# Kernel optimization log

Measured on AMD Instinct MI355X. Metric: run time of the kernel, lower is better.

The kernel has to match this reference:

```python
import jax, jax.numpy as jnp
import numpy as np

LN_EPS = 1e-5
N_HEADS = 8

def _layernorm(x, g, b):
    mu = jnp.mean(x, axis=-1, keepdims=True)
    var = jnp.var(x, axis=-1, keepdims=True)
    return (x - mu) * jax.lax.rsqrt(var + LN_EPS) * g + b

def _posenc(seqlen, d_model, dtype):
    den = jnp.exp(-jnp.arange(0, d_model, 2, dtype=dtype) * (np.log(10000.0) / d_model))
    pos = jnp.arange(seqlen, dtype=dtype)[:, None]  # [S,1]
    pe = jnp.zeros((seqlen, d_model), dtype=dtype)
    pe = pe.at[:, 0::2].set(jnp.sin(pos * den))
    pe = pe.at[:, 1::2].set(jnp.cos(pos * den)[:, : d_model // 2])
    return pe  # [S,d]

def setup_inputs() -> dict:
    key = jax.random.key(0)
    ks = jax.random.split(key, 12)
    B, S, V, D, F, L, DL = 64, 256, 16, 512, 2048, 6, 256
    s = 0.05
    return {
        "src_pad": jax.random.normal(ks[0], (B, S, V), jnp.float32),
        "emb_w": jax.random.normal(ks[1], (D, V), jnp.float32) * s,
        "emb_b": jnp.zeros((D,), jnp.float32),
        "qkv_w": jax.random.normal(ks[2], (L, 3 * D, D), jnp.float32) * s,
        "qkv_b": jnp.zeros((L, 3 * D), jnp.float32),
        "out_w": jax.random.normal(ks[3], (L, D, D), jnp.float32) * s,
        "out_b": jnp.zeros((L, D), jnp.float32),
        "ff1_w": jax.random.normal(ks[4], (L, F, D), jnp.float32) * s,
        "ff1_b": jnp.zeros((L, F), jnp.float32),
        "ff2_w": jax.random.normal(ks[5], (L, D, F), jnp.float32) * s,
        "ff2_b": jnp.zeros((L, D), jnp.float32),
        "ln1_g": jnp.ones((L, D), jnp.float32),
        "ln1_b": jnp.zeros((L, D), jnp.float32),
        "ln2_g": jnp.ones((L, D), jnp.float32),
        "ln2_b": jnp.zeros((L, D), jnp.float32),
        "lat_w": jax.random.normal(ks[6], (DL, S * D), jnp.float32) * 0.005,
        "lat_b": jnp.zeros((DL,), jnp.float32),
        "head_w": jax.random.normal(ks[7], (1, DL), jnp.float32) * s,
        "head_b": jnp.zeros((1,), jnp.float32),
    }

def reference(src_pad, emb_w, emb_b, qkv_w, qkv_b, out_w, out_b,
              ff1_w, ff1_b, ff2_w, ff2_b, ln1_g, ln1_b, ln2_g, ln2_b,
              lat_w, lat_b, head_w, head_b):
    B, S, V = src_pad.shape
    D = emb_w.shape[0]
    L = qkv_w.shape[0]
    H = N_HEADS
    dh = D // H
    # batched replacement of the per-token Python-loop embedding
    x = jnp.einsum('bsv,dv->bsd', src_pad, emb_w) + emb_b
    x = x + _posenc(S, D, x.dtype)  # dropout is identity at eval
    scale = 1.0 / np.sqrt(dh)
    for l in range(L):  # post-norm PyTorch TransformerEncoderLayer, relu FFN
        qkv = jnp.einsum('bsd,ed->bse', x, qkv_w[l]) + qkv_b[l]  # [B,S,3D]
        q, k, v = jnp.split(qkv, 3, axis=-1)
        q = q.reshape(B, S, H, dh).transpose(0, 2, 1, 3)
        k = k.reshape(B, S, H, dh).transpose(0, 2, 1, 3)
        v = v.reshape(B, S, H, dh).transpose(0, 2, 1, 3)
        attn = jax.nn.softmax(jnp.einsum('bhqd,bhkd->bhqk', q, k) * scale, axis=-1)
        o = jnp.einsum('bhqk,bhkd->bhqd', attn, v).transpose(0, 2, 1, 3).reshape(B, S, D)
        o = jnp.einsum('bsd,ed->bse', o, out_w[l]) + out_b[l]
        x = _layernorm(x + o, ln1_g[l], ln1_b[l])
        h = jax.nn.relu(jnp.einsum('bsd,fd->bsf', x, ff1_w[l]) + ff1_b[l])
        h = jnp.einsum('bsf,df->bsd', h, ff2_w[l]) + ff2_b[l]
        x = _layernorm(x + h, ln2_g[l], ln2_b[l])
    mem = x.reshape(B, S * D) @ lat_w.T + lat_b  # [B, d_latent]
    pred = jax.nn.sigmoid(mem @ head_w.T + head_b)  # [B,1]
    return pred
```

## Files before the change

### kernel.cpp

```cpp
#include <hip/hip_runtime.h>
#include <hip/hip_bf16.h>
#include <cstdint>

#define DEV static __device__ __forceinline__

typedef __attribute__((ext_vector_type(8))) short bf16x8;
typedef __attribute__((ext_vector_type(4))) float f32x4;

DEV unsigned short f2bf(float f) {
  union { float f; unsigned u; } c; c.f = f;
  unsigned u = c.u;
  return (unsigned short)((u + 0x7fffu + ((u >> 16) & 1u)) >> 16);
}
DEV float bf2f(unsigned short h) {
  union { unsigned u; float f; } c; c.u = ((unsigned)h) << 16; return c.f;
}
DEV float bflo(unsigned u) { union { unsigned u; float f; } c; c.u = u << 16; return c.f; }
DEV float bfhi(unsigned u) { union { unsigned u; float f; } c; c.u = u & 0xffff0000u; return c.f; }
DEV unsigned pack_bf16(float a, float b) {
  union { float f; unsigned u; } ca, cb; ca.f = a; cb.f = b;
  return __builtin_amdgcn_perm(cb.u + 0x8000u, ca.u + 0x8000u, 0x07060302u);
}

#define ASYNC_COPY16(gsrc, ldst)                                                      \
  __builtin_amdgcn_global_load_lds(                                                   \
      (const __attribute__((address_space(1))) void*)(unsigned long long)(gsrc),      \
      (__attribute__((address_space(3))) void*)(unsigned int)(unsigned long long)(ldst), \
      16, 0, 0)

__global__ void cvt4_kernel(const float* __restrict__ s, unsigned short* __restrict__ d) {
  size_t i = ((size_t)blockIdx.x * 256 + threadIdx.x) * 4;
  float4 v = *(const float4*)(s + i);
  d[i + 0] = f2bf(v.x);
  d[i + 1] = f2bf(v.y);
  d[i + 2] = f2bf(v.z);
  d[i + 3] = f2bf(v.w);
}

__global__ void embed_kernel(const float* __restrict__ src,
                             const float* __restrict__ emb_w,
                             const float* __restrict__ emb_b,
                             unsigned short* __restrict__ xb) {
  const int bs = blockIdx.x;
  const int d = threadIdx.x;
  const int s = bs & 255;
  __shared__ float sv[16];
  if (d < 16) sv[d] = src[(size_t)bs * 16 + d];
  __syncthreads();
  const float* wr = emb_w + (size_t)d * 16;
  float acc = emb_b[d];
#pragma unroll
  for (int v = 0; v < 16; v++) acc += sv[v] * wr[v];
  const float den = __expf(-(float)(d & ~1) * (9.2103403719761836f / 512.f));
  const float arg = (float)s * den;
  acc += (d & 1) ? __cosf(arg) : __sinf(arg);
  xb[(size_t)bs * 512 + d] = f2bf(acc);
}

template <int BM, int RELU, int OUT_BF16, int ADD_RES>
__global__ __launch_bounds__(512, 2) void gemm_pipe(
    const unsigned short* __restrict__ A,
    const unsigned short* __restrict__ B,
    const float* __restrict__ bias,
    const unsigned short* __restrict__ res,
    float* __restrict__ Cf,
    unsigned short* __restrict__ Cb,
    int M, int N, int K) {
  constexpr int BN = 256;
  constexpr int MT = BM / 32;
  constexpr int NT = 4;
  constexpr int NLA = BM / 64;
  constexpr int NL = NLA + 4;
  __shared__ unsigned short lds[2][(BM + BN) * 64];

  const int tid = threadIdx.x;
  const int lane = tid & 63;
  const int w = tid >> 6;
  const int wmi = w >> 2;
  const int wni = w & 3;
  const int r16 = lane & 15;
  const int quad = lane >> 4;
  const int rsw = r16 & 7;
  const int m0 = blockIdx.x * BM;
  const int n0 = blockIdx.y * BN;

  const int srow = tid >> 3;
  const int scol = ((tid & 7) ^ (srow & 7)) * 8;
  const unsigned short* gA = A + (size_t)(m0 + srow) * K + scol;
  const unsigned short* gB = B + (size_t)(n0 + srow) * K + scol;

#define STG(i, bufi, kc)                                                        \
  do {                                                                          \
    if ((i) < NLA)                                                              \
      ASYNC_COPY16(gA + (size_t)((i) * 64) * K + (kc),                          \
                   &lds[(bufi)][((i) * 64 + w * 8) * 64]);                      \
    else                                                                        \
      ASYNC_COPY16(gB + (size_t)(((i) - NLA) * 64) * K + (kc),                  \
                   &lds[(bufi)][(BM + ((i) - NLA) * 64 + w * 8) * 64]);         \
  } while (0)

  f32x4 acc[MT][NT] = {};

#pragma unroll
  for (int i = 0; i < NL; ++i) STG(i, 0, 0);

  const int NK = K >> 6;
  for (int kt = 0; kt < NK; ++kt) {
    const int buf = kt & 1;
    asm volatile("s_waitcnt vmcnt(0)" ::: "memory");
    __builtin_amdgcn_s_barrier();
    const unsigned short* As = &lds[buf][0];
    const unsigned short* Bs = &lds[buf][BM * 64];
    const int doStage = (kt + 1 < NK);
    const int kc = (kt + 1) << 6;
    const int sb = buf ^ 1;
    bf16x8 aR[MT];
#pragma unroll
    for (int kh = 0; kh < 2; ++kh) {
#pragma unroll
      for (int nh = 0; nh < 2; ++nh) {
        const int ph = kh * 2 + nh;
        const int ko = ((kh * 4 + quad) ^ rsw) * 8;
        if (nh == 0) {
#pragma unroll
          for (int m = 0; m < MT; ++m)
            aR[m] = *(const bf16x8*)(As + (wmi * (MT * 16) + m * 16 + r16) * 64 + ko);
        }
        bf16x8 bR[2];
#pragma unroll
        for (int j = 0; j < 2; ++j)
          bR[j] = *(const bf16x8*)(Bs + (wni * 64 + (nh * 2 + j) * 16 + r16) * 64 + ko);
        if (doStage) {
          if (2 * ph < NL) STG(2 * ph, sb, kc);
          if (2 * ph + 1 < NL) STG(2 * ph + 1, sb, kc);
        }
        __builtin_amdgcn_s_barrier();
        asm volatile("s_waitcnt lgkmcnt(0)" ::: "memory");
        __builtin_amdgcn_s_setprio(1);
#pragma unroll
        for (int m = 0; m < MT; ++m)
#pragma unroll
          for (int j = 0; j < 2; ++j)
            acc[m][nh * 2 + j] = __builtin_amdgcn_mfma_f32_16x16x32_bf16(
                bR[j], aR[m], acc[m][nh * 2 + j], 0, 0, 0);
        __builtin_amdgcn_s_setprio(0);
        __builtin_amdgcn_s_barrier();
      }
    }
  }
#undef STG

  const int mb = m0 + wmi * (MT * 16) + r16;
  const int nb = n0 + wni * 64 + quad * 4;
#pragma unroll
  for (int j = 0; j < NT; ++j) {
    const int n = nb + j * 16;
    const float4 bv = *(const float4*)(bias + n);
#pragma unroll
    for (int i = 0; i < MT; ++i) {
      const size_t off = (size_t)(mb + i * 16) * N + n;
      float4 v;
      v.x = acc[i][j][0] + bv.x;
      v.y = acc[i][j][1] + bv.y;
      v.z = acc[i][j][2] + bv.z;
      v.w = acc[i][j][3] + bv.w;
      if (ADD_RES) {
        const uint2 ru = *(const uint2*)(res + off);
        v.x += bflo(ru.x); v.y += bfhi(ru.x);
        v.z += bflo(ru.y); v.w += bfhi(ru.y);
      }
      if (RELU) {
        v.x = fmaxf(v.x, 0.f); v.y = fmaxf(v.y, 0.f);
        v.z = fmaxf(v.z, 0.f); v.w = fmaxf(v.w, 0.f);
      }
      if (OUT_BF16) {
        uint2 u;
        u.x = pack_bf16(v.x, v.y);
        u.y = pack_bf16(v.z, v.w);
        *(uint2*)(Cb + off) = u;
      } else {
        *(float4*)(Cf + off) = v;
      }
    }
  }
}

__global__ __launch_bounds__(256, 2) void attn_fused(
    const unsigned short* __restrict__ qkv,
    unsigned short* __restrict__ O) {
  __shared__ unsigned short Vt[64 * 264];
  __shared__ unsigned short Pl[32 * 264];
  __shared__ float redM[4][32];
  __shared__ float redS[4][32];
  const int tid = threadIdx.x;
  const int lane = tid & 63;
  const int w = tid >> 6;
  const int r16 = lane & 15;
  const int quad = lane >> 4;
  const int h = blockIdx.x & 7;
  const int b = blockIdx.x >> 3;

  {
    const int kp = w * 32 + (lane & 31);
    const int dhalf = lane >> 5;
    const unsigned short* vbase =
        qkv + (size_t)(b * 256 + 2 * kp) * 1536 + 1024 + h * 64;
    unsigned* dst = (unsigned*)Vt;
#pragma unroll
    for (int t = 0; t < 4; t++) {
      const int dc = dhalf + 2 * t;
      const uint4 a = *(const uint4*)(vbase + dc * 8);
      const uint4 bb = *(const uint4*)(vbase + 1536 + dc * 8);
      const unsigned* ap = (const unsigned*)&a;
      const unsigned* bp = (const unsigned*)&bb;
#pragma unroll
      for (int i = 0; i < 4; i++) {
        const unsigned lo = ap[i], hi = bp[i];
        dst[(dc * 8 + 2 * i) * 132 + kp] = (lo & 0xffffu) | (hi << 16);
        dst[(dc * 8 + 2 * i + 1) * 132 + kp] = (lo >> 16) | (hi & 0xffff0000u);
      }
    }
  }
  __syncthreads();

  const unsigned short* krow =
      qkv + (size_t)(b * 256 + r16) * 1536 + 512 + h * 64 + quad * 8;
  const unsigned short* qrow =
      qkv + (size_t)(b * 256 + r16) * 1536 + h * 64 + quad * 8;

  for (int qt = 0; qt < 8; qt++) {
    const int q0 = qt * 32;
    f32x4 acc[4][2] = {};
    bf16x8 bQ0[2], bQ1[2];
#pragma unroll
    for (int nt = 0; nt < 2; nt++) {
      const unsigned short* qp = qrow + (size_t)(q0 + nt * 16) * 1536;
      bQ0[nt] = *(const bf16x8*)(qp);
      bQ1[nt] = *(const bf16x8*)(qp + 32);
    }
#pragma unroll
    for (int mt = 0; mt < 4; mt++) {
      const unsigned short* kp = krow + (size_t)(w * 64 + mt * 16) * 1536;
      const bf16x8 aK0 = *(const bf16x8*)(kp);
      const bf16x8 aK1 = *(const bf16x8*)(kp + 32);
#pragma unroll
      for (int nt = 0; nt < 2; nt++) {
        acc[mt][nt] = __builtin_amdgcn_mfma_f32_16x16x32_bf16(aK0, bQ0[nt], acc[mt][nt], 0, 0, 0);
        acc[mt][nt] = __builtin_amdgcn_mfma_f32_16x16x32_bf16(aK1, bQ1[nt], acc[mt][nt], 0, 0, 0);
      }
    }
#pragma unroll
    for (int nt = 0; nt < 2; nt++) {
      float m = acc[0][nt][0];
#pragma unroll
      for (int mt = 0; mt < 4; mt++)
#pragma unroll
        for (int r = 0; r < 4; r++) m = fmaxf(m, acc[mt][nt][r]);
      m = fmaxf(m, __shfl_xor(m, 16));
      m = fmaxf(m, __shfl_xor(m, 32));
      if (quad == 0) redM[w][nt * 16 + r16] = m;
    }
    __syncthreads();
    float mg[2], sw[2];
#pragma unroll
    for (int nt = 0; nt < 2; nt++) {
      const int q = nt * 16 + r16;
      mg[nt] = fmaxf(fmaxf(redM[0][q], redM[1][q]), fmaxf(redM[2][q], redM[3][q]));
      sw[nt] = 0.f;
    }
#pragma unroll
    for (int mt = 0; mt < 4; mt++)
#pragma unroll
      for (int nt = 0; nt < 2; nt++)
#pragma unroll
        for (int r = 0; r < 4; r++) {
          acc[mt][nt][r] = __expf((acc[mt][nt][r] - mg[nt]) * 0.125f);
          sw[nt] += acc[mt][nt][r];
        }
#pragma unroll
    for (int nt = 0; nt < 2; nt++) {
      sw[nt] += __shfl_xor(sw[nt], 16);
      sw[nt] += __shfl_xor(sw[nt], 32);
      if (quad == 0) redS[w][nt * 16 + r16] = sw[nt];
    }
    __syncthreads();
    float inv[2];
#pragma unroll
    for (int nt = 0; nt < 2; nt++) {
      const int q = nt * 16 + r16;
      inv[nt] = 1.f / (redS[0][q] + redS[1][q] + redS[2][q] + redS[3][q]);
    }
#pragma unroll
    for (int nt = 0; nt < 2; nt++) {
      unsigned short* prow = Pl + (nt * 16 + r16) * 264 + w * 64 + quad * 4;
#pragma unroll
      for (int mt = 0; mt < 4; mt++) {
        uint2 u;
        u.x = pack_bf16(acc[mt][nt][0] * inv[nt], acc[mt][nt][1] * inv[nt]);
        u.y = pack_bf16(acc[mt][nt][2] * inv[nt], acc[mt][nt][3] * inv[nt]);
        *(uint2*)(prow + mt * 16) = u;
      }
    }
    __syncthreads();
    f32x4 o[2] = {};
#pragma unroll
    for (int s = 0; s < 8; s++) {
      const bf16x8 aV = *(const bf16x8*)(Vt + (w * 16 + r16) * 264 + s * 32 + quad * 8);
#pragma unroll
      for (int nt = 0; nt < 2; nt++) {
        const bf16x8 bP = *(const bf16x8*)(Pl + (nt * 16 + r16) * 264 + s * 32 + quad * 8);
        o[nt] = __builtin_amdgcn_mfma_f32_16x16x32_bf16(aV, bP, o[nt], 0, 0, 0);
      }
    }
#pragma unroll
    for (int nt = 0; nt < 2; nt++) {
      uint2 u;
      u.x = pack_bf16(o[nt][0], o[nt][1]);
      u.y = pack_bf16(o[nt][2], o[nt][3]);
      *(uint2*)(O + (size_t)(b * 256 + q0 + nt * 16 + r16) * 512 + h * 64 +
                w * 16 + quad * 4) = u;
    }
  }
}

__global__ __launch_bounds__(256) void ln_kernel(
    const float* __restrict__ z, const float* __restrict__ g,
    const float* __restrict__ bb, unsigned short* __restrict__ xb) {
  const int row = blockIdx.x;
  const int tid = threadIdx.x;
  const size_t base = (size_t)row * 512;
  float v0 = z[base + tid];
  float v1 = z[base + tid + 256];
  float s = v0 + v1, ss = v0 * v0 + v1 * v1;
#pragma unroll
  for (int off = 32; off > 0; off >>= 1) {
    s += __shfl_xor(s, off);
    ss += __shfl_xor(ss, off);
  }
  __shared__ float red[8];
  const int w = tid >> 6, lane = tid & 63;
  if (lane == 0) { red[w * 2] = s; red[w * 2 + 1] = ss; }
  __syncthreads();
  s = red[0] + red[2] + red[4] + red[6];
  ss = red[1] + red[3] + red[5] + red[7];
  const float mu = s * (1.f / 512.f);
  const float var = ss * (1.f / 512.f) - mu * mu;
  const float rs = rsqrtf(var + 1e-5f);
  const float o0 = (v0 - mu) * rs * g[tid] + bb[tid];
  const float o1 = (v1 - mu) * rs * g[tid + 256] + bb[tid + 256];
  xb[base + tid] = f2bf(o0);
  xb[base + tid + 256] = f2bf(o1);
}

__global__ void zero_kernel(float* __restrict__ p) {
  p[blockIdx.x * 256 + threadIdx.x] = 0.f;
}

__global__ __launch_bounds__(256) void latent_gemm(
    const unsigned short* __restrict__ xb, const float* __restrict__ W,
    float* __restrict__ mem) {
  const int tid = threadIdx.x;
  const int lane = tid & 63;
  const int w = tid >> 6;
  const int r16 = lane & 15;
  const int quad = lane >> 4;
  const int n0 = blockIdx.x * 64 + w * 16;
  const int kc0 = blockIdx.y * 1024;

  const float* wrow = W + (size_t)(n0 + r16) * 131072 + kc0 + quad * 8;
  const unsigned short* xrow = xb + (size_t)r16 * 131072 + kc0 + quad * 8;

  f32x4 c[4] = {};
  for (int k = 0; k < 1024; k += 32) {
    const float4 wa = *(const float4*)(wrow + k);
    const float4 wb = *(const float4*)(wrow + k + 4);
    union { unsigned u[4]; bf16x8 v; } cw;
    cw.u[0] = pack_bf16(wa.x, wa.y);
    cw.u[1] = pack_bf16(wa.z, wa.w);
    cw.u[2] = pack_bf16(wb.x, wb.y);
    cw.u[3] = pack_bf16(wb.z, wb.w);
#pragma unroll
    for (int i = 0; i < 4; i++) {
      const bf16x8 aX = *(const bf16x8*)(xrow + (size_t)i * 2097152 + k);
      c[i] = __builtin_amdgcn_mfma_f32_16x16x32_bf16(aX, cw.v, c[i], 0, 0, 0);
    }
  }
#pragma unroll
  for (int i = 0; i < 4; i++)
#pragma unroll
    for (int r = 0; r < 4; r++)
      atomicAdd(&mem[(size_t)(i * 16 + quad * 4 + r) * 256 + n0 + r16], c[i][r]);
}

__global__ __launch_bounds__(256) void head_kernel(
    const float* __restrict__ mem, const float* __restrict__ lat_b,
    const float* __restrict__ head_w, const float* __restrict__ head_b,
    float* __restrict__ out) {
  const int b = blockIdx.x;
  const int tid = threadIdx.x;
  float v = (mem[(size_t)b * 256 + tid] + lat_b[tid]) * head_w[tid];
#pragma unroll
  for (int off = 32; off > 0; off >>= 1) v += __shfl_xor(v, off);
  __shared__ float red[4];
  const int w = tid >> 6, lane = tid & 63;
  if (lane == 0) red[w] = v;
  __syncthreads();
  if (tid == 0) {
    const float z = red[0] + red[1] + red[2] + red[3] + head_b[0];
    out[b] = 1.f / (1.f + __expf(-z));
  }
}

extern "C" void kernel_launch(void* const* d_in, const int* in_sizes, int n_in,
                              void* d_out, int out_size, void* d_ws, size_t ws_size,
                              hipStream_t stream) {
  (void)in_sizes; (void)n_in; (void)out_size; (void)ws_size;
  const float* src_pad = (const float*)d_in[0];
  const float* emb_w = (const float*)d_in[1];
  const float* emb_b = (const float*)d_in[2];
  const float* qkv_w = (const float*)d_in[3];
  const float* qkv_b = (const float*)d_in[4];
  const float* out_w = (const float*)d_in[5];
  const float* out_b = (const float*)d_in[6];
  const float* ff1_w = (const float*)d_in[7];
  const float* ff1_b = (const float*)d_in[8];
  const float* ff2_w = (const float*)d_in[9];
  const float* ff2_b = (const float*)d_in[10];
  const float* ln1_g = (const float*)d_in[11];
  const float* ln1_b = (const float*)d_in[12];
  const float* ln2_g = (const float*)d_in[13];
  const float* ln2_b = (const float*)d_in[14];
  const float* lat_w = (const float*)d_in[15];
  const float* lat_b = (const float*)d_in[16];
  const float* head_w = (const float*)d_in[17];
  const float* head_b = (const float*)d_in[18];
  float* out = (float*)d_out;

  char* p = (char*)d_ws;
  unsigned short* xb = (unsigned short*)p; p += (size_t)16384 * 512 * 2;
  unsigned short* qkv = (unsigned short*)p;
  float* y = (float*)qkv;
  p += (size_t)16384 * 1536 * 2;
  unsigned short* attno = (unsigned short*)p; p += (size_t)16384 * 512 * 2;
  unsigned short* h = (unsigned short*)p;     p += (size_t)16384 * 2048 * 2;
  unsigned short* wq = (unsigned short*)p;    p += (size_t)4718592 * 2;
  unsigned short* wo = (unsigned short*)p;    p += (size_t)1572864 * 2;
  unsigned short* wf1 = (unsigned short*)p;   p += (size_t)6291456 * 2;
  unsigned short* wf2 = (unsigned short*)p;   p += (size_t)6291456 * 2;
  float* mem = (float*)p;           p += (size_t)16384 * 4;

  cvt4_kernel<<<4608, 256, 0, stream>>>(qkv_w, wq);
  cvt4_kernel<<<1536, 256, 0, stream>>>(out_w, wo);
  cvt4_kernel<<<6144, 256, 0, stream>>>(ff1_w, wf1);
  cvt4_kernel<<<6144, 256, 0, stream>>>(ff2_w, wf2);

  embed_kernel<<<16384, 512, 0, stream>>>(src_pad, emb_w, emb_b, xb);

  for (int l = 0; l < 6; l++) {
    gemm_pipe<128, 0, 1, 0><<<dim3(128, 6), 512, 0, stream>>>(
        xb, wq + (size_t)l * 786432, qkv_b + (size_t)l * 1536, nullptr,
        nullptr, qkv, 16384, 1536, 512);
    attn_fused<<<512, 256, 0, stream>>>(qkv, attno);
    gemm_pipe<128, 0, 0, 1><<<dim3(128, 2), 512, 0, stream>>>(
        attno, wo + (size_t)l * 262144, out_b + (size_t)l * 512, xb,
        y, nullptr, 16384, 512, 512);
    ln_kernel<<<16384, 256, 0, stream>>>(y, ln1_g + (size_t)l * 512,
                                         ln1_b + (size_t)l * 512, xb);
    gemm_pipe<256, 1, 1, 0><<<dim3(64, 8), 512, 0, stream>>>(
        xb, wf1 + (size_t)l * 1048576, ff1_b + (size_t)l * 2048, nullptr,
        nullptr, h, 16384, 2048, 512);
    gemm_pipe<128, 0, 0, 1><<<dim3(128, 2), 512, 0, stream>>>(
        h, wf2 + (size_t)l * 1048576, ff2_b + (size_t)l * 512, xb,
        y, nullptr, 16384, 512, 2048);
    ln_kernel<<<16384, 256, 0, stream>>>(y, ln2_g + (size_t)l * 512,
                                         ln2_b + (size_t)l * 512, xb);
  }

  zero_kernel<<<64, 256, 0, stream>>>(mem);
  latent_gemm<<<dim3(4, 128), 256, 0, stream>>>(xb, lat_w, mem);
  head_kernel<<<64, 256, 0, stream>>>(mem, lat_b, head_w, head_b, out);
}
```

Measured before the change: 1.652 ms.

## Triple-buffer GEMM LDS pipeline and drop per-phase barriers

The bf16 MFMA GEMM now uses three LDS stages instead of two. It prefetches two k-tiles ahead and waits with a partial vmcnt, so only the oldest outstanding tile has to arrive before compute starts. The inner loop is simplified to one barrier per k-tile: all A and B fragments are loaded per k-half, with no interleaved staging and no barriers per sub-phase. The FF1 GEMM switches from a 256-row tile to a 128-row tile with twice as many blocks. The trade-offs are about 144KB of LDS per block, more registers held per phase, and the code now assuming BM=128.

```diff
diff --git a/kernel.cpp b/kernel.cpp
--- a/kernel.cpp
+++ b/kernel.cpp
@@ -70,8 +70,9 @@
   constexpr int MT = BM / 32;
   constexpr int NT = 4;
   constexpr int NLA = BM / 64;
-  constexpr int NL = NLA + 4;
-  __shared__ unsigned short lds[2][(BM + BN) * 64];
+  constexpr int NL = NLA + BN / 64;
+  constexpr int BUFE = (BM + BN) * 64;
+  __shared__ unsigned short lds[3 * BUFE];
 
   const int tid = threadIdx.x;
   const int lane = tid & 63;
@@ -93,64 +94,59 @@
   do {                                                                          \
     if ((i) < NLA)                                                              \
       ASYNC_COPY16(gA + (size_t)((i) * 64) * K + (kc),                          \
-                   &lds[(bufi)][((i) * 64 + w * 8) * 64]);                      \
+                   lds + (bufi) * BUFE + ((i) * 64 + w * 8) * 64);              \
     else                                                                        \
       ASYNC_COPY16(gB + (size_t)(((i) - NLA) * 64) * K + (kc),                  \
-                   &lds[(bufi)][(BM + ((i) - NLA) * 64 + w * 8) * 64]);         \
+                   lds + (bufi) * BUFE + (BM + ((i) - NLA) * 64 + w * 8) * 64); \
   } while (0)
 
   f32x4 acc[MT][NT] = {};
 
+  const int NK = K >> 6;
 #pragma unroll
   for (int i = 0; i < NL; ++i) STG(i, 0, 0);
-
-  const int NK = K >> 6;
+#pragma unroll
+  for (int i = 0; i < NL; ++i) STG(i, 1, 64);
+
   for (int kt = 0; kt < NK; ++kt) {
-    const int buf = kt & 1;
-    asm volatile("s_waitcnt vmcnt(0)" ::: "memory");
+    const int buf = kt % 3;
+    if (kt + 1 < NK)
+      asm volatile("s_waitcnt vmcnt(%0)" ::"i"(NL) : "memory");
+    else
+      asm volatile("s_waitcnt vmcnt(0)" ::: "memory");
     __builtin_amdgcn_s_barrier();
-    const unsigned short* As = &lds[buf][0];
-    const unsigned short* Bs = &lds[buf][BM * 64];
-    const int doStage = (kt + 1 < NK);
-    const int kc = (kt + 1) << 6;
-    const int sb = buf ^ 1;
-    bf16x8 aR[MT];
+    if (kt + 2 < NK) {
+      const int sb = (kt + 2) % 3;
+      const int kc = (kt + 2) << 6;
+#pragma unroll
+      for (int i = 0; i < NL; ++i) STG(i, sb, kc);
+    }
+    const unsigned short* As = lds + buf * BUFE;
+    const unsigned short* Bs = As + BM * 64;
 #pragma unroll
     for (int kh = 0; kh < 2; ++kh) {
-#pragma unroll
-      for (int nh = 0; nh < 2; ++nh) {
-        const int ph = kh * 2 + nh;
-        const int ko = ((kh * 4 + quad) ^ rsw) * 8;
-        if (nh == 0) {
-#pragma unroll
-          for (int m = 0; m < MT; ++m)
-            aR[m] = *(const bf16x8*)(As + (wmi * (MT * 16) + m * 16 + r16) * 64 + ko);
-        }
-        bf16x8 bR[2];
-#pragma unroll
-        for (int j = 0; j < 2; ++j)
-          bR[j] = *(const bf16x8*)(Bs + (wni * 64 + (nh * 2 + j) * 16 + r16) * 64 + ko);
-        if (doStage) {
-          if (2 * ph < NL) STG(2 * ph, sb, kc);
-          if (2 * ph + 1 < NL) STG(2 * ph + 1, sb, kc);
-        }
-        __builtin_amdgcn_s_barrier();
-        asm volatile("s_waitcnt lgkmcnt(0)" ::: "memory");
-        __builtin_amdgcn_s_setprio(1);
-#pragma unroll
-        for (int m = 0; m < MT; ++m)
-#pragma unroll
-          for (int j = 0; j < 2; ++j)
-            acc[m][nh * 2 + j] = __builtin_amdgcn_mfma_f32_16x16x32_bf16(
-                bR[j], aR[m], acc[m][nh * 2 + j], 0, 0, 0);
-        __builtin_amdgcn_s_setprio(0);
-        __builtin_amdgcn_s_barrier();
-      }
-    }
+      const int ko = ((kh * 4 + quad) ^ rsw) * 8;
+      bf16x8 aR[MT], bR[NT];
+#pragma unroll
+      for (int m = 0; m < MT; ++m)
+        aR[m] = *(const bf16x8*)(As + (wmi * 64 + m * 16 + r16) * 64 + ko);
+#pragma unroll
+      for (int j = 0; j < NT; ++j)
+        bR[j] = *(const bf16x8*)(Bs + (wni * 64 + j * 16 + r16) * 64 + ko);
+      __builtin_amdgcn_s_setprio(1);
+#pragma unroll
+      for (int m = 0; m < MT; ++m)
+#pragma unroll
+        for (int j = 0; j < NT; ++j)
+          acc[m][j] = __builtin_amdgcn_mfma_f32_16x16x32_bf16(
+              bR[j], aR[m], acc[m][j], 0, 0, 0);
+      __builtin_amdgcn_s_setprio(0);
+    }
+    asm volatile("s_waitcnt lgkmcnt(0)" ::: "memory");
   }
 #undef STG
 
-  const int mb = m0 + wmi * (MT * 16) + r16;
+  const int mb = m0 + wmi * 64 + r16;
   const int nb = n0 + wni * 64 + quad * 4;
 #pragma unroll
   for (int j = 0; j < NT; ++j) {
@@ -466,7 +462,7 @@
         y, nullptr, 16384, 512, 512);
     ln_kernel<<<16384, 256, 0, stream>>>(y, ln1_g + (size_t)l * 512,
                                          ln1_b + (size_t)l * 512, xb);
-    gemm_pipe<256, 1, 1, 0><<<dim3(64, 8), 512, 0, stream>>>(
+    gemm_pipe<128, 1, 1, 0><<<dim3(128, 8), 512, 0, stream>>>(
         xb, wf1 + (size_t)l * 1048576, ff1_b + (size_t)l * 2048, nullptr,
         nullptr, h, 16384, 2048, 512);
     gemm_pipe<128, 0, 0, 1><<<dim3(128, 2), 512, 0, stream>>>(
```

Result: faster. 1.584 ms (-4.1%).
